# Optimization experiments

Measured on AMD Instinct MI355X. Metric: run time of the kernel, lower is better.

Reference implementation:

```python
import jax, jax.numpy as jnp
import numpy as np

V, D, E, N, Dd, Dc, NL, B, L = 50280, 1024, 2048, 16, 64, 4, 2, 2, 1024
EPS = 1e-5


def rmsnorm(x, w):
    return x * jax.lax.rsqrt(jnp.mean(x * x, axis=-1, keepdims=True) + EPS) * w


def setup_inputs() -> dict:
    key = jax.random.key(0)
    ks = jax.random.split(key, 18)
    n = jax.random.normal
    inp = {
        "input_ids": jax.random.randint(ks[0], (B, L), 0, V),
        "embedding": n(ks[1], (V, D), jnp.float32) * 0.02,
        "lm_head_w": n(ks[2], (V, D), jnp.float32) * 0.02,
        "norm_w": jnp.ones((D,), jnp.float32),
        # stacked per-layer params (leading dim = n_layer)
        "l_norm_w": jnp.ones((NL, D), jnp.float32),
        "l_skip_w": n(ks[3], (NL, E, D), jnp.float32) / np.sqrt(D),
        "l_in_w": n(ks[4], (NL, E, D), jnp.float32) / np.sqrt(D),
        "l_conv_w": n(ks[5], (NL, E, 1, Dc), jnp.float32) / np.sqrt(Dc),
        "l_conv_b": jnp.zeros((NL, E), jnp.float32),
        "l_Wd1": n(ks[6], (NL, Dd, E), jnp.float32) / np.sqrt(E),
        "l_Wd2_w": n(ks[7], (NL, E, Dd), jnp.float32) / np.sqrt(Dd),
        "l_Wd2_b": n(ks[8], (NL, E), jnp.float32) * 0.1 - 4.0,  # small dt init
        "l_WB": n(ks[9], (NL, N, E), jnp.float32) / np.sqrt(E),
        "l_WC": n(ks[10], (NL, N, E), jnp.float32) / np.sqrt(E),
        "l_A_log": jnp.log(jax.random.uniform(ks[11], (NL, E, N), jnp.float32, 0.5, 1.2)),
        "l_WD": jnp.ones((NL, E), jnp.float32),
        "l_out_w": n(ks[12], (NL, D, E), jnp.float32) / np.sqrt(E),
    }
    return inp


def mamba_layer(resid, norm_w, skip_w, in_w, conv_w, conv_b, Wd1, Wd2_w, Wd2_b,
                WB, WC, A_log, WD, out_w):
    x = rmsnorm(resid, norm_w)                      # [B,L,D]
    skip = x @ skip_w.T                             # [B,L,E]
    x = x @ in_w.T                                  # [B,L,E]
    # depthwise causal conv (pad D_conv-1 on left == pad both + slice [:L])
    xc = jax.lax.conv_general_dilated(
        x.transpose(0, 2, 1), conv_w, (1,), [(Dc - 1, 0)],
        feature_group_count=E, dimension_numbers=("NCH", "OIH", "NCH"))
    x = (xc + conv_b[None, :, None]).transpose(0, 2, 1)  # [B,L,E]
    x = jax.nn.silu(x)

    delta = jax.nn.softplus((x @ Wd1.T) @ Wd2_w.T + Wd2_b)  # [B,L,E]
    A = -jnp.exp(A_log)                                      # [E,N]
    A_bar = jnp.exp(delta[..., None] * A)                    # [B,L,E,N]
    Bt = x @ WB.T                                            # [B,L,N]
    Ct = x @ WC.T                                            # [B,L,N]
    Bx = (delta * x)[..., None] * Bt[:, :, None, :]          # [B,L,E,N]

    def step(h, inp):
        Ab_t, Bx_t, C_t = inp                                # [B,E,N],[B,E,N],[B,N]
        h = Ab_t * h + Bx_t
        y = jnp.einsum("ben,bn->be", h, C_t)
        return h, y

    h0 = jnp.zeros((B, E, N), x.dtype)
    _, ys = jax.lax.scan(step, h0,
                         (A_bar.transpose(1, 0, 2, 3), Bx.transpose(1, 0, 2, 3),
                          Ct.transpose(1, 0, 2)))
    y = ys.transpose(1, 0, 2)                                # [B,L,E]
    y = y + x * WD
    y = y * jax.nn.silu(skip)
    return resid + y @ out_w.T


def reference(input_ids, embedding, lm_head_w, norm_w, l_norm_w, l_skip_w, l_in_w,
              l_conv_w, l_conv_b, l_Wd1, l_Wd2_w, l_Wd2_b, l_WB, l_WC, l_A_log,
              l_WD, l_out_w):
    resid = embedding[input_ids]                             # [B,L,D]
    for i in range(NL):
        resid = mamba_layer(resid, l_norm_w[i], l_skip_w[i], l_in_w[i],
                            l_conv_w[i], l_conv_b[i], l_Wd1[i], l_Wd2_w[i],
                            l_Wd2_b[i], l_WB[i], l_WC[i], l_A_log[i], l_WD[i],
                            l_out_w[i])
    resid = rmsnorm(resid, norm_w)
    return resid @ lm_head_w.T                               # [B,L,V]
```

## Files before the change

### kernel.cpp

```cpp
#include <hip/hip_runtime.h>

typedef unsigned short u16;
using bf16x8 = __attribute__((ext_vector_type(8))) __bf16;
using f32x4  = __attribute__((ext_vector_type(4))) float;

typedef const void __attribute__((address_space(1))) gvoid_t;
typedef void __attribute__((address_space(3))) lvoid_t;

#define NL 2
#define Bd 2
#define Ld 1024
#define Dd_ 1024
#define Ed 2048
#define Nd 16
#define TOK (Bd*Ld)
#define VPAD 50432
#define VREAL 50280
#define NCHUNK 8
#define CLEN 128
#define XLD 4096

__device__ __forceinline__ u16 f2bf(float f) {
    union { float f; unsigned u; } v; v.f = f;
    unsigned u = v.u;
    unsigned r = (u + 0x7fffu + ((u >> 16) & 1u)) >> 16;
    return (u16)r;
}
__device__ __forceinline__ float siluf(float x) { return x / (1.f + __expf(-x)); }
__device__ __forceinline__ float softplusf(float z) {
    return (z > 15.f) ? z : log1pf(__expf(z));
}

__global__ void k_f32_to_bf16(const float* __restrict__ s, u16* __restrict__ d, int n4) {
    int i = blockIdx.x * 256 + threadIdx.x;
    if (i >= n4) return;
    float4 v = *(const float4*)&s[(size_t)i * 4];
    ushort4 o; o.x = f2bf(v.x); o.y = f2bf(v.y); o.z = f2bf(v.z); o.w = f2bf(v.w);
    *(ushort4*)&d[(size_t)i * 4] = o;
}

__global__ void k_f32_to_bf16_pad(const float* __restrict__ s, u16* __restrict__ d,
                                  int n4valid, int n4tot) {
    int i = blockIdx.x * 256 + threadIdx.x;
    if (i >= n4tot) return;
    ushort4 o;
    if (i < n4valid) {
        float4 v = *(const float4*)&s[(size_t)i * 4];
        o.x = f2bf(v.x); o.y = f2bf(v.y); o.z = f2bf(v.z); o.w = f2bf(v.w);
    } else { o.x = o.y = o.z = o.w = 0; }
    *(ushort4*)&d[(size_t)i * 4] = o;
}

__global__ void k_build_wsmall(const float* __restrict__ Wd1, const float* __restrict__ WB,
                               const float* __restrict__ WC, u16* __restrict__ dst) {
    int i = blockIdx.x * 256 + threadIdx.x;
    int col = (i * 4) & (Ed - 1);
    int r = (i * 4) >> 11;
    ushort4 o;
    const float* src = nullptr;
    if (r < 64) src = &Wd1[(size_t)r * Ed];
    else if (r < 80) src = &WB[(size_t)(r - 64) * Ed];
    else if (r < 96) src = &WC[(size_t)(r - 80) * Ed];
    if (src) {
        float4 v = *(const float4*)&src[col];
        o.x = f2bf(v.x); o.y = f2bf(v.y); o.z = f2bf(v.z); o.w = f2bf(v.w);
    } else { o.x = o.y = o.z = o.w = 0; }
    *(ushort4*)&dst[(size_t)i * 4] = o;
}

__global__ void k_embed(const int* __restrict__ ids, const float* __restrict__ emb,
                        float* __restrict__ resid) {
    int tk = blockIdx.x;
    int d = threadIdx.x * 4;
    int id = ids[tk];
    float4 v = *(const float4*)&emb[(size_t)id * Dd_ + d];
    *(float4*)&resid[(size_t)tk * Dd_ + d] = v;
}

__global__ void k_rmsnorm_bf16(const float* __restrict__ in, const float* __restrict__ w,
                               u16* __restrict__ out) {
    int tk = blockIdx.x;
    int tid = threadIdx.x;
    float4 v = *(const float4*)&in[(size_t)tk * Dd_ + tid * 4];
    float ss = v.x * v.x + v.y * v.y + v.z * v.z + v.w * v.w;
    #pragma unroll
    for (int m = 32; m; m >>= 1) ss += __shfl_xor(ss, m);
    __shared__ float red[4];
    if ((tid & 63) == 0) red[tid >> 6] = ss;
    __syncthreads();
    ss = red[0] + red[1] + red[2] + red[3];
    float rs = rsqrtf(ss * (1.f / 1024.f) + 1e-5f);
    float4 wv = *(const float4*)&w[tid * 4];
    ushort4 o;
    o.x = f2bf(v.x * rs * wv.x); o.y = f2bf(v.y * rs * wv.y);
    o.z = f2bf(v.z * rs * wv.z); o.w = f2bf(v.w * rs * wv.w);
    *(ushort4*)&out[(size_t)tk * Dd_ + tid * 4] = o;
}

__global__ void k_conv_silu(const float* __restrict__ xin, const float* __restrict__ cw,
                            const float* __restrict__ cb, float* __restrict__ xout,
                            u16* __restrict__ xbf) {
    int blk = blockIdx.x;
    int tk = blk >> 1;
    int e0 = ((blk & 1) << 10) + threadIdx.x * 4;
    int b = tk >> 10, l = tk & 1023;
    float4 w0 = *(const float4*)&cw[(size_t)(e0 + 0) * 4];
    float4 w1 = *(const float4*)&cw[(size_t)(e0 + 1) * 4];
    float4 w2 = *(const float4*)&cw[(size_t)(e0 + 2) * 4];
    float4 w3 = *(const float4*)&cw[(size_t)(e0 + 3) * 4];
    float4 bv = *(const float4*)&cb[e0];
    float a0 = bv.x, a1 = bv.y, a2 = bv.z, a3 = bv.w;
    const float* wp0 = (const float*)&w0; const float* wp1 = (const float*)&w1;
    const float* wp2 = (const float*)&w2; const float* wp3 = (const float*)&w3;
    #pragma unroll
    for (int k = 0; k < 4; ++k) {
        int ll = l - 3 + k;
        if (ll < 0) continue;
        float4 xv = *(const float4*)&xin[((size_t)(b * 1024 + ll)) * XLD + e0];
        a0 = fmaf(xv.x, wp0[k], a0); a1 = fmaf(xv.y, wp1[k], a1);
        a2 = fmaf(xv.z, wp2[k], a2); a3 = fmaf(xv.w, wp3[k], a3);
    }
    a0 = siluf(a0); a1 = siluf(a1); a2 = siluf(a2); a3 = siluf(a3);
    float4 o; o.x = a0; o.y = a1; o.z = a2; o.w = a3;
    *(float4*)&xout[(size_t)tk * Ed + e0] = o;
    ushort4 ob; ob.x = f2bf(a0); ob.y = f2bf(a1); ob.z = f2bf(a2); ob.w = f2bf(a3);
    *(ushort4*)&xbf[(size_t)tk * Ed + e0] = ob;
}

__global__ void k_reduce_xs(const float* __restrict__ part, float* __restrict__ xs,
                            u16* __restrict__ xsbf) {
    size_t i4 = ((size_t)blockIdx.x * 256 + threadIdx.x) * 4;
    float4 s = *(const float4*)&part[i4];
    #pragma unroll
    for (int c = 1; c < NCHUNK; ++c) {
        float4 v = *(const float4*)&part[(size_t)c * TOK * 128 + i4];
        s.x += v.x; s.y += v.y; s.z += v.z; s.w += v.w;
    }
    *(float4*)&xs[i4] = s;
    ushort4 o; o.x = f2bf(s.x); o.y = f2bf(s.y); o.z = f2bf(s.z); o.w = f2bf(s.w);
    *(ushort4*)&xsbf[i4] = o;
}

__global__ void k_scan_pass1(const float* __restrict__ delta, const float* __restrict__ x,
                             const float* __restrict__ xs, const float* __restrict__ A_log,
                             float* __restrict__ sumd, float* __restrict__ Hc) {
    int t = blockIdx.x * 256 + threadIdx.x;
    int n = t & 15;
    int gg = t >> 4;
    int e = gg & (Ed - 1);
    int cb = gg >> 11;
    int b = cb & 1, c = cb >> 1;
    float dA = -__expf(A_log[e * Nd + n]);
    float h = 0.f, sd = 0.f;
    size_t rowbase = ((size_t)b << 10) + c * CLEN;
    for (int l = 0; l < CLEN; ++l) {
        size_t row = rowbase + l;
        float dlt = delta[row * Ed + e];
        float xv  = x[row * Ed + e];
        float bt  = xs[row * 128 + 64 + n];
        float a = __expf(dA * dlt);
        h = fmaf(a, h, dlt * xv * bt);
        sd += dlt;
    }
    Hc[(size_t)gg * Nd + n] = h;
    if (n == 0) sumd[gg] = sd;
}

__global__ void k_scan_combine(const float* __restrict__ sumd, const float* __restrict__ Hc,
                               const float* __restrict__ A_log, float* __restrict__ Hin) {
    int idx = blockIdx.x * 256 + threadIdx.x;
    int n = idx & 15;
    int e = (idx >> 4) & (Ed - 1);
    int b = idx >> 15;
    float dA = -__expf(A_log[e * Nd + n]);
    float h = 0.f;
    #pragma unroll
    for (int c = 0; c < NCHUNK; ++c) {
        size_t g = ((size_t)(c * Bd + b) * Ed + e);
        Hin[g * Nd + n] = h;
        float a = __expf(dA * sumd[g]);
        h = fmaf(a, h, Hc[g * Nd + n]);
    }
}

__global__ void k_scan_pass2(const float* __restrict__ delta, const float* __restrict__ x,
                             const float* __restrict__ xs, const float* __restrict__ A_log,
                             const float* __restrict__ Hin, const float* __restrict__ WD,
                             const float* __restrict__ skipg, u16* __restrict__ ybf) {
    int t = blockIdx.x * 256 + threadIdx.x;
    int n = t & 15;
    int gg = t >> 4;
    int e = gg & (Ed - 1);
    int cb = gg >> 11;
    int b = cb & 1, c = cb >> 1;
    float dA = -__expf(A_log[e * Nd + n]);
    float h = Hin[(size_t)gg * Nd + n];
    float wd = WD[e];
    size_t rowbase = ((size_t)b << 10) + c * CLEN;
    for (int l = 0; l < CLEN; ++l) {
        size_t row = rowbase + l;
        float dlt = delta[row * Ed + e];
        float xv  = x[row * Ed + e];
        float bt  = xs[row * 128 + 64 + n];
        float ct  = xs[row * 128 + 80 + n];
        float a = __expf(dA * dlt);
        h = fmaf(a, h, dlt * xv * bt);
        float yv = h * ct;
        yv += __shfl_xor(yv, 1);
        yv += __shfl_xor(yv, 2);
        yv += __shfl_xor(yv, 4);
        yv += __shfl_xor(yv, 8);
        if (n == 0) {
            float yo = yv + xv * wd;
            float sk = skipg[row * XLD + e];
            ybf[row * Ed + e] = f2bf(yo * siluf(sk));
        }
    }
}

template<int EPI>
__global__ __launch_bounds__(256, 2)
void k_gemm_bt(const u16* __restrict__ A, int lda,
               const u16* __restrict__ B, int ldb,
               float* __restrict__ C, int ldc,
               const float* __restrict__ aux,
               int ntm, int Nstore, int Kc, size_t Cz) {
    __shared__ u16 lsA[2][128 * 32];
    __shared__ u16 lsB[2][128 * 32];
    int kz = blockIdx.z;
    A += (size_t)kz * Kc;
    B += (size_t)kz * Kc;
    C += (size_t)kz * Cz;
    int tid = threadIdx.x;
    int bid = blockIdx.x;
    int mt = bid % ntm, nt = bid / ntm;
    int mBase = mt * 128, nBase = nt * 128;
    int lane = tid & 63, wid = tid >> 6;
    int wr = wid >> 1, wc = wid & 1;

    f32x4 acc[4][4] = {};
    const u16* Ablk = A + (size_t)mBase * lda;
    const u16* Bblk = B + (size_t)nBase * ldb;
    int nk = Kc >> 5;

    auto stage = [&](int buf, int kt) {
        #pragma unroll
        for (int i = 0; i < 2; ++i) {
            int chunk = i * 256 + tid;
            int row = chunk >> 2;
            int kc  = (chunk & 3) << 3;
            const u16* ga = Ablk + (size_t)row * lda + (kt << 5) + kc;
            const u16* gb = Bblk + (size_t)row * ldb + (kt << 5) + kc;
            u16* la = &lsA[buf][(size_t)(i * 256 + wid * 64) * 8];
            u16* lb = &lsB[buf][(size_t)(i * 256 + wid * 64) * 8];
            __builtin_amdgcn_global_load_lds((gvoid_t*)ga, (lvoid_t*)la, 16, 0, 0);
            __builtin_amdgcn_global_load_lds((gvoid_t*)gb, (lvoid_t*)lb, 16, 0, 0);
        }
    };
    auto compute = [&](int buf) {
        bf16x8 af[4], bfr[4];
        const u16* baseA = lsA[buf];
        const u16* baseB = lsB[buf];
        int kq = (lane >> 4) << 3;
        int r  = lane & 15;
        #pragma unroll
        for (int mi = 0; mi < 4; ++mi)
            af[mi] = *(const bf16x8*)&baseA[(size_t)((wr * 64 + mi * 16 + r) * 32 + kq)];
        #pragma unroll
        for (int ni = 0; ni < 4; ++ni)
            bfr[ni] = *(const bf16x8*)&baseB[(size_t)((wc * 64 + ni * 16 + r) * 32 + kq)];
        #pragma unroll
        for (int mi = 0; mi < 4; ++mi)
            #pragma unroll
            for (int ni = 0; ni < 4; ++ni)
                acc[mi][ni] = __builtin_amdgcn_mfma_f32_16x16x32_bf16(af[mi], bfr[ni], acc[mi][ni], 0, 0, 0);
    };

    stage(0, 0);
    asm volatile("s_waitcnt vmcnt(0)" ::: "memory");
    __syncthreads();
    int cur = 0;
    for (int kt = 0; kt + 1 < nk; ++kt) {
        stage(cur ^ 1, kt + 1);
        compute(cur);
        asm volatile("s_waitcnt vmcnt(0)" ::: "memory");
        __syncthreads();
        cur ^= 1;
    }
    compute(cur);

    int rbase = (lane >> 4) * 4, ccol = lane & 15;
    #pragma unroll
    for (int mi = 0; mi < 4; ++mi) {
        #pragma unroll
        for (int ni = 0; ni < 4; ++ni) {
            int gc = nBase + wc * 64 + ni * 16 + ccol;
            if (gc < Nstore) {
                float bias = (EPI == 2) ? aux[gc] : 0.f;
                #pragma unroll
                for (int rr = 0; rr < 4; ++rr) {
                    int gr = mBase + wr * 64 + mi * 16 + rbase + rr;
                    size_t off = (size_t)gr * ldc + gc;
                    float v = acc[mi][ni][rr];
                    if (EPI == 1) v += aux[off];
                    if (EPI == 2) v = softplusf(v + bias);
                    C[off] = v;
                }
            }
        }
    }
}

#define BAR()    asm volatile("s_barrier" ::: "memory")
#define WAITV2() asm volatile("s_waitcnt vmcnt(2)" ::: "memory")
#define WAITV0() asm volatile("s_waitcnt vmcnt(0)" ::: "memory")

#define STG(buf, mat, h, kt) { \
    const u16* _s0 = ((mat) ? srcB[(h)*2]     : srcA[(h)*2])     + (size_t)(kt) * 64; \
    const u16* _s1 = ((mat) ? srcB[(h)*2 + 1] : srcA[(h)*2 + 1]) + (size_t)(kt) * 64; \
    char* _d = (char*)&ls[buf][mat][0]; \
    __builtin_amdgcn_global_load_lds((gvoid_t*)_s0, (lvoid_t*)(_d + (h)*16384 + tid*16), 16, 0, 0); \
    __builtin_amdgcn_global_load_lds((gvoid_t*)_s1, (lvoid_t*)(_d + (h)*16384 + 8192 + tid*16), 16, 0, 0); }

#define QUAD(buf, kk, mih) { \
    const char* _pa = (const char*)&ls[buf][0][0]; \
    const char* _pb = (const char*)&ls[buf][1][0]; \
    bf16x8 _af[4], _bf[4]; \
    _Pragma("unroll") \
    for (int _m = 0; _m < 4; ++_m) \
        _af[_m] = *(const bf16x8*)(_pa + abase + ((mih)*4 + _m) * 2048 + (kk) * 1024); \
    _Pragma("unroll") \
    for (int _n = 0; _n < 4; ++_n) \
        _bf[_n] = *(const bf16x8*)(_pb + bbase + _n * 2048 + (kk) * 1024); \
    __builtin_amdgcn_s_setprio(1); \
    _Pragma("unroll") \
    for (int _m = 0; _m < 4; ++_m) \
        _Pragma("unroll") \
        for (int _n = 0; _n < 4; ++_n) \
            acc[(mih)*4 + _m][_n] = __builtin_amdgcn_mfma_f32_16x16x32_bf16(_af[_m], _bf[_n], acc[(mih)*4 + _m][_n], 0, 0, 0); \
    __builtin_amdgcn_s_setprio(0); }

__global__ __launch_bounds__(512, 2)
void k_gemm256(const u16* __restrict__ A, int lda,
               const u16* __restrict__ B, int ldb,
               float* __restrict__ C, int ldc,
               int ntm, int Nstore, int K) {
    __shared__ u16 ls[2][2][256 * 64];
    const int tid = threadIdx.x;
    const int lane = tid & 63, wid = tid >> 6;
    const int wr = wid >> 2, wc = wid & 3;

    int nwg = gridDim.x, bid = blockIdx.x;
    int q8 = nwg >> 3, r8 = nwg & 7;
    int xcd = bid & 7, linb = bid >> 3;
    int sb = (xcd < r8 ? xcd * (q8 + 1) : r8 * (q8 + 1) + (xcd - r8) * q8) + linb;
    int mt = sb % ntm, nt = sb / ntm;

    const u16* Ablk = A + (size_t)(mt * 256) * lda;
    const u16* Bblk = B + (size_t)(nt * 256) * ldb;

    const u16* srcA[4]; const u16* srcB[4];
    #pragma unroll
    for (int s = 0; s < 4; ++s) {
        int p = s * 8192 + tid * 16;
        int qq = p ^ (((p >> 9) & 1) << 5);
        int sub = qq >> 10, rin = (qq >> 6) & 15, cby = qq & 63;
        int row = ((sub >> 1) << 4) | rin;
        int col = ((((sub & 1) << 6) | cby)) >> 1;
        srcA[s] = Ablk + (size_t)row * lda + col;
        srcB[s] = Bblk + (size_t)row * ldb + col;
    }
    int l15 = lane & 15;
    int lowb = (l15 * 64 + ((lane >> 4) << 4)) ^ (((l15 >> 3) & 1) << 5);
    int abase = wr * 16384 + lowb;
    int bbase = wc * 8192  + lowb;

    f32x4 acc[8][4] = {};
    int nk = K >> 6, nit = nk >> 1;

    STG(0, 0, 0, 0); STG(0, 0, 1, 0); STG(0, 1, 0, 0); STG(0, 1, 1, 0);

    for (int i = 0; i < nit; ++i) {
        int t1 = 2 * i + 1, t2 = 2 * i + 2;
        bool more = (i + 1 < nit);
        STG(1, 0, 0, t1);
        WAITV2(); BAR();
        QUAD(0, 0, 0); BAR();
        STG(1, 0, 1, t1);
        QUAD(0, 0, 1); BAR();
        STG(1, 1, 0, t1);
        QUAD(0, 1, 0); BAR();
        STG(1, 1, 1, t1);
        QUAD(0, 1, 1); BAR();
        if (more) { STG(0, 0, 0, t2); WAITV2(); } else { WAITV0(); }
        BAR();
        QUAD(1, 0, 0); BAR();
        if (more) STG(0, 0, 1, t2);
        QUAD(1, 0, 1); BAR();
        if (more) STG(0, 1, 0, t2);
        QUAD(1, 1, 0); BAR();
        if (more) STG(0, 1, 1, t2);
        QUAD(1, 1, 1); BAR();
    }

    int rb = (lane >> 4) * 4, cc = lane & 15;
    int mrow = mt * 256 + wr * 128, ncol = nt * 256 + wc * 64;
    #pragma unroll
    for (int mi = 0; mi < 8; ++mi) {
        #pragma unroll
        for (int ni = 0; ni < 4; ++ni) {
            int gc = ncol + ni * 16 + cc;
            if (gc < Nstore) {
                #pragma unroll
                for (int rr = 0; rr < 4; ++rr) {
                    size_t off = (size_t)(mrow + mi * 16 + rb + rr) * ldc + gc;
                    C[off] = acc[mi][ni][rr];
                }
            }
        }
    }
}

extern "C" void kernel_launch(void* const* d_in, const int* in_sizes, int n_in,
                              void* d_out, int out_size, void* d_ws, size_t ws_size,
                              hipStream_t stream) {
    const int*   ids   = (const int*)d_in[0];
    const float* emb   = (const float*)d_in[1];
    const float* lmw   = (const float*)d_in[2];
    const float* normw = (const float*)d_in[3];
    const float* lnw   = (const float*)d_in[4];
    const float* lskip = (const float*)d_in[5];
    const float* linw  = (const float*)d_in[6];
    const float* lcw   = (const float*)d_in[7];
    const float* lcb   = (const float*)d_in[8];
    const float* lWd1  = (const float*)d_in[9];
    const float* lWd2  = (const float*)d_in[10];
    const float* lWd2b = (const float*)d_in[11];
    const float* lWB   = (const float*)d_in[12];
    const float* lWC   = (const float*)d_in[13];
    const float* lAlog = (const float*)d_in[14];
    const float* lWD   = (const float*)d_in[15];
    const float* loutw = (const float*)d_in[16];
    float* out = (float*)d_out;

    char* ws = (char*)d_ws;
    size_t off = 0;
    auto alloc = [&](size_t bytes) { char* p = ws + off; off += (bytes + 255) & ~(size_t)255; return p; };
    u16*   lm_bf    = (u16*)  alloc((size_t)VPAD * 1024 * 2);
    u16*   wsi_bf   = (u16*)  alloc((size_t)NL * 4096 * Dd_ * 2);
    u16*   wout_bf  = (u16*)  alloc((size_t)NL * Dd_ * Ed * 2);
    u16*   wd2_bf   = (u16*)  alloc((size_t)NL * Ed * 64 * 2);
    u16*   wsml_bf  = (u16*)  alloc((size_t)NL * 128 * Ed * 2);
    float* resid    = (float*)alloc((size_t)TOK * Dd_ * 4);
    u16*   xn_bf    = (u16*)  alloc((size_t)TOK * Dd_ * 2);
    float* xall     = (float*)alloc((size_t)TOK * XLD * 4);
    float* xf       = (float*)alloc((size_t)TOK * Ed * 4);
    u16*   xbf      = (u16*)  alloc((size_t)TOK * Ed * 2);
    float* xs       = (float*)alloc((size_t)TOK * 128 * 4);
    u16*   xs_bf    = (u16*)  alloc((size_t)TOK * 128 * 2);
    float* xs_part  = (float*)alloc((size_t)NCHUNK * TOK * 128 * 4);
    float* delta    = (float*)alloc((size_t)TOK * Ed * 4);
    float* sumd     = (float*)alloc((size_t)NCHUNK * Bd * Ed * 4);
    float* Hc       = (float*)alloc((size_t)NCHUNK * Bd * Ed * Nd * 4);
    float* Hin      = (float*)alloc((size_t)NCHUNK * Bd * Ed * Nd * 4);
    u16*   ybf      = (u16*)  alloc((size_t)TOK * Ed * 2);
    (void)ws_size; (void)in_sizes; (void)n_in; (void)out_size;

    {
        int n4v = VREAL * 1024 / 4, n4t = VPAD * 1024 / 4;
        k_f32_to_bf16_pad<<<(n4t + 255) / 256, 256, 0, stream>>>(lmw, lm_bf, n4v, n4t);
        int n4 = Ed * Dd_ / 4;
        for (int lyr = 0; lyr < NL; ++lyr) {
            k_f32_to_bf16<<<(n4 + 255) / 256, 256, 0, stream>>>(
                lskip + (size_t)lyr * Ed * Dd_, wsi_bf + (size_t)lyr * 4096 * Dd_, n4);
            k_f32_to_bf16<<<(n4 + 255) / 256, 256, 0, stream>>>(
                linw + (size_t)lyr * Ed * Dd_, wsi_bf + (size_t)lyr * 4096 * Dd_ + (size_t)Ed * Dd_, n4);
        }
        k_f32_to_bf16<<<(NL * n4 + 255) / 256, 256, 0, stream>>>(loutw, wout_bf, NL * n4);
        int n4b = NL * Ed * 64 / 4;
        k_f32_to_bf16<<<(n4b + 255) / 256, 256, 0, stream>>>(lWd2, wd2_bf, n4b);
        for (int lyr = 0; lyr < NL; ++lyr)
            k_build_wsmall<<<256, 256, 0, stream>>>(lWd1 + (size_t)lyr * 64 * Ed,
                                                    lWB + (size_t)lyr * Nd * Ed,
                                                    lWC + (size_t)lyr * Nd * Ed,
                                                    wsml_bf + (size_t)lyr * 128 * Ed);
    }

    k_embed<<<TOK, 256, 0, stream>>>(ids, emb, resid);

    for (int lyr = 0; lyr < NL; ++lyr) {
        const float* Alog = lAlog + (size_t)lyr * Ed * Nd;
        k_rmsnorm_bf16<<<TOK, 256, 0, stream>>>(resid, lnw + (size_t)lyr * Dd_, xn_bf);
        k_gemm_bt<0><<<dim3(16 * 32, 1, 1), 256, 0, stream>>>(xn_bf, Dd_,
            wsi_bf + (size_t)lyr * 4096 * Dd_, Dd_, xall, XLD, nullptr, 16, 4096, 1024, 0);
        k_conv_silu<<<TOK * 2, 256, 0, stream>>>(xall + Ed, lcw + (size_t)lyr * Ed * 4,
                                                 lcb + (size_t)lyr * Ed, xf, xbf);
        k_gemm_bt<0><<<dim3(16, 1, NCHUNK), 256, 0, stream>>>(xbf, Ed,
            wsml_bf + (size_t)lyr * 128 * Ed, Ed, xs_part, 128, nullptr, 16, 128, 256,
            (size_t)TOK * 128);
        k_reduce_xs<<<TOK * 128 / 4 / 256, 256, 0, stream>>>(xs_part, xs, xs_bf);
        k_gemm_bt<2><<<dim3(16 * 16, 1, 1), 256, 0, stream>>>(xs_bf, 128,
            wd2_bf + (size_t)lyr * Ed * 64, 64, delta, Ed, lWd2b + (size_t)lyr * Ed,
            16, Ed, 64, 0);
        k_scan_pass1<<<NCHUNK * Bd * Ed * Nd / 256, 256, 0, stream>>>(delta, xf, xs, Alog, sumd, Hc);
        k_scan_combine<<<Bd * Ed * Nd / 256, 256, 0, stream>>>(sumd, Hc, Alog, Hin);
        k_scan_pass2<<<NCHUNK * Bd * Ed * Nd / 256, 256, 0, stream>>>(delta, xf, xs, Alog, Hin,
            lWD + (size_t)lyr * Ed, xall, ybf);
        k_gemm_bt<1><<<dim3(16 * 8, 1, 1), 256, 0, stream>>>(ybf, Ed,
            wout_bf + (size_t)lyr * Dd_ * Ed, Ed, resid, Dd_, resid, 16, Dd_, 2048, 0);
    }

    k_rmsnorm_bf16<<<TOK, 256, 0, stream>>>(resid, normw, xn_bf);
    k_gemm256<<<dim3(8 * (VPAD / 256), 1, 1), 512, 0, stream>>>(xn_bf, Dd_, lm_bf, Dd_,
        out, VREAL, 8, VREAL, 1024);
}
```

Baseline: 943.2 us.

## Restructure selective scan to one thread per channel and reshape lm_head pipeline

The scan kernels switch from sixteen threads per channel, which reduced the output with shuffles, to one thread per channel that keeps all 16 state values in registers. Each block stages B/C rows in shared memory, and the chunk count doubles to 16 chunks of 64 steps to keep enough threads in flight. The xs split-K reduction is decoupled and stays at 8. Separately, the big lm_head GEMM's inner loop now issues twice as many LDS loads and MFMAs per stage between barriers, with a looser vmcnt wait. This cuts barrier count but raises register pressure.

```diff
diff --git a/kernel.cpp b/kernel.cpp
--- a/kernel.cpp
+++ b/kernel.cpp
@@ -16,8 +16,8 @@
 #define TOK (Bd*Ld)
 #define VPAD 50432
 #define VREAL 50280
-#define NCHUNK 8
-#define CLEN 128
+#define NCHUNK 16
+#define CLEN 64
 #define XLD 4096
 
 __device__ __forceinline__ u16 f2bf(float f) {
@@ -132,7 +132,7 @@
     size_t i4 = ((size_t)blockIdx.x * 256 + threadIdx.x) * 4;
     float4 s = *(const float4*)&part[i4];
     #pragma unroll
-    for (int c = 1; c < NCHUNK; ++c) {
+    for (int c = 1; c < 8; ++c) {
         float4 v = *(const float4*)&part[(size_t)c * TOK * 128 + i4];
         s.x += v.x; s.y += v.y; s.z += v.z; s.w += v.w;
     }
@@ -144,26 +144,47 @@
 __global__ void k_scan_pass1(const float* __restrict__ delta, const float* __restrict__ x,
                              const float* __restrict__ xs, const float* __restrict__ A_log,
                              float* __restrict__ sumd, float* __restrict__ Hc) {
+    __shared__ float sBt[CLEN][16];
     int t = blockIdx.x * 256 + threadIdx.x;
-    int n = t & 15;
-    int gg = t >> 4;
-    int e = gg & (Ed - 1);
-    int cb = gg >> 11;
+    int e = t & (Ed - 1);
+    int cb = t >> 11;
     int b = cb & 1, c = cb >> 1;
-    float dA = -__expf(A_log[e * Nd + n]);
-    float h = 0.f, sd = 0.f;
-    size_t rowbase = ((size_t)b << 10) + c * CLEN;
+    int rowbase = b * 1024 + c * CLEN;
+    {
+        int f = threadIdx.x * 4;
+        int row = f >> 4, cc = f & 15;
+        float4 v = *(const float4*)&xs[(size_t)(rowbase + row) * 128 + 64 + cc];
+        *(float4*)&sBt[row][cc] = v;
+    }
+    __syncthreads();
+    float dA[16], h[16];
+    #pragma unroll
+    for (int n = 0; n < 16; ++n) { dA[n] = -__expf(A_log[e * 16 + n]); h[n] = 0.f; }
+    float sd = 0.f;
     for (int l = 0; l < CLEN; ++l) {
-        size_t row = rowbase + l;
+        size_t row = (size_t)rowbase + l;
         float dlt = delta[row * Ed + e];
         float xv  = x[row * Ed + e];
-        float bt  = xs[row * 128 + 64 + n];
-        float a = __expf(dA * dlt);
-        h = fmaf(a, h, dlt * xv * bt);
         sd += dlt;
-    }
-    Hc[(size_t)gg * Nd + n] = h;
-    if (n == 0) sumd[gg] = sd;
+        float dx = dlt * xv;
+        float4 bt0 = *(const float4*)&sBt[l][0];
+        float4 bt1 = *(const float4*)&sBt[l][4];
+        float4 bt2 = *(const float4*)&sBt[l][8];
+        float4 bt3 = *(const float4*)&sBt[l][12];
+        const float* btp = (const float*)&bt0;
+        float bts[16] = {bt0.x,bt0.y,bt0.z,bt0.w, bt1.x,bt1.y,bt1.z,bt1.w,
+                         bt2.x,bt2.y,bt2.z,bt2.w, bt3.x,bt3.y,bt3.z,bt3.w};
+        (void)btp;
+        #pragma unroll
+        for (int n = 0; n < 16; ++n) {
+            float a = __expf(dA[n] * dlt);
+            h[n] = fmaf(a, h[n], dx * bts[n]);
+        }
+    }
+    size_t gg = (size_t)cb * Ed + e;
+    #pragma unroll
+    for (int n = 0; n < 16; ++n) Hc[gg * 16 + n] = h[n];
+    sumd[gg] = sd;
 }
 
 __global__ void k_scan_combine(const float* __restrict__ sumd, const float* __restrict__ Hc,
@@ -187,34 +208,56 @@
                              const float* __restrict__ xs, const float* __restrict__ A_log,
                              const float* __restrict__ Hin, const float* __restrict__ WD,
                              const float* __restrict__ skipg, u16* __restrict__ ybf) {
+    __shared__ float sBC[CLEN][32];
     int t = blockIdx.x * 256 + threadIdx.x;
-    int n = t & 15;
-    int gg = t >> 4;
-    int e = gg & (Ed - 1);
-    int cb = gg >> 11;
+    int e = t & (Ed - 1);
+    int cb = t >> 11;
     int b = cb & 1, c = cb >> 1;
-    float dA = -__expf(A_log[e * Nd + n]);
-    float h = Hin[(size_t)gg * Nd + n];
+    int rowbase = b * 1024 + c * CLEN;
+    {
+        int f = threadIdx.x * 8;
+        int row = f >> 5, cc = f & 31;
+        float4 v0 = *(const float4*)&xs[(size_t)(rowbase + row) * 128 + 64 + cc];
+        float4 v1 = *(const float4*)&xs[(size_t)(rowbase + row) * 128 + 64 + cc + 4];
+        *(float4*)&sBC[row][cc] = v0;
+        *(float4*)&sBC[row][cc + 4] = v1;
+    }
+    __syncthreads();
+    float dA[16], h[16];
+    size_t gg = (size_t)cb * Ed + e;
+    #pragma unroll
+    for (int n = 0; n < 16; ++n) {
+        dA[n] = -__expf(A_log[e * 16 + n]);
+        h[n] = Hin[gg * 16 + n];
+    }
     float wd = WD[e];
-    size_t rowbase = ((size_t)b << 10) + c * CLEN;
     for (int l = 0; l < CLEN; ++l) {
-        size_t row = rowbase + l;
+        size_t row = (size_t)rowbase + l;
         float dlt = delta[row * Ed + e];
         float xv  = x[row * Ed + e];
-        float bt  = xs[row * 128 + 64 + n];
-        float ct  = xs[row * 128 + 80 + n];
-        float a = __expf(dA * dlt);
-        h = fmaf(a, h, dlt * xv * bt);
-        float yv = h * ct;
-        yv += __shfl_xor(yv, 1);
-        yv += __shfl_xor(yv, 2);
-        yv += __shfl_xor(yv, 4);
-        yv += __shfl_xor(yv, 8);
-        if (n == 0) {
-            float yo = yv + xv * wd;
-            float sk = skipg[row * XLD + e];
-            ybf[row * Ed + e] = f2bf(yo * siluf(sk));
+        float dx = dlt * xv;
+        float4 b0 = *(const float4*)&sBC[l][0];
+        float4 b1 = *(const float4*)&sBC[l][4];
+        float4 b2 = *(const float4*)&sBC[l][8];
+        float4 b3 = *(const float4*)&sBC[l][12];
+        float4 c0 = *(const float4*)&sBC[l][16];
+        float4 c1 = *(const float4*)&sBC[l][20];
+        float4 c2 = *(const float4*)&sBC[l][24];
+        float4 c3 = *(const float4*)&sBC[l][28];
+        float bts[16] = {b0.x,b0.y,b0.z,b0.w, b1.x,b1.y,b1.z,b1.w,
+                         b2.x,b2.y,b2.z,b2.w, b3.x,b3.y,b3.z,b3.w};
+        float cts[16] = {c0.x,c0.y,c0.z,c0.w, c1.x,c1.y,c1.z,c1.w,
+                         c2.x,c2.y,c2.z,c2.w, c3.x,c3.y,c3.z,c3.w};
+        float y = 0.f;
+        #pragma unroll
+        for (int n = 0; n < 16; ++n) {
+            float a = __expf(dA[n] * dlt);
+            h[n] = fmaf(a, h[n], dx * bts[n]);
+            y = fmaf(h[n], cts[n], y);
         }
+        float yo = y + xv * wd;
+        float sk = skipg[row * XLD + e];
+        ybf[row * Ed + e] = f2bf(yo * siluf(sk));
     }
 }
 
@@ -312,7 +355,7 @@
 }
 
 #define BAR()    asm volatile("s_barrier" ::: "memory")
-#define WAITV2() asm volatile("s_waitcnt vmcnt(2)" ::: "memory")
+#define WAITV4() asm volatile("s_waitcnt vmcnt(4)" ::: "memory")
 #define WAITV0() asm volatile("s_waitcnt vmcnt(0)" ::: "memory")
 
 #define STG(buf, mat, h, kt) { \
@@ -322,22 +365,22 @@
     __builtin_amdgcn_global_load_lds((gvoid_t*)_s0, (lvoid_t*)(_d + (h)*16384 + tid*16), 16, 0, 0); \
     __builtin_amdgcn_global_load_lds((gvoid_t*)_s1, (lvoid_t*)(_d + (h)*16384 + 8192 + tid*16), 16, 0, 0); }
 
-#define QUAD(buf, kk, mih) { \
+#define KSLICE(buf, kk) { \
     const char* _pa = (const char*)&ls[buf][0][0]; \
     const char* _pb = (const char*)&ls[buf][1][0]; \
-    bf16x8 _af[4], _bf[4]; \
+    bf16x8 _af[8], _bf[4]; \
     _Pragma("unroll") \
-    for (int _m = 0; _m < 4; ++_m) \
-        _af[_m] = *(const bf16x8*)(_pa + abase + ((mih)*4 + _m) * 2048 + (kk) * 1024); \
+    for (int _m = 0; _m < 8; ++_m) \
+        _af[_m] = *(const bf16x8*)(_pa + abase + _m * 2048 + (kk) * 1024); \
     _Pragma("unroll") \
     for (int _n = 0; _n < 4; ++_n) \
         _bf[_n] = *(const bf16x8*)(_pb + bbase + _n * 2048 + (kk) * 1024); \
     __builtin_amdgcn_s_setprio(1); \
     _Pragma("unroll") \
-    for (int _m = 0; _m < 4; ++_m) \
+    for (int _m = 0; _m < 8; ++_m) \
         _Pragma("unroll") \
         for (int _n = 0; _n < 4; ++_n) \
-            acc[(mih)*4 + _m][_n] = __builtin_amdgcn_mfma_f32_16x16x32_bf16(_af[_m], _bf[_n], acc[(mih)*4 + _m][_n], 0, 0, 0); \
+            acc[_m][_n] = __builtin_amdgcn_mfma_f32_16x16x32_bf16(_af[_m], _bf[_n], acc[_m][_n], 0, 0, 0); \
     __builtin_amdgcn_s_setprio(0); }
 
 __global__ __launch_bounds__(512, 2)
@@ -383,24 +426,16 @@
     for (int i = 0; i < nit; ++i) {
         int t1 = 2 * i + 1, t2 = 2 * i + 2;
         bool more = (i + 1 < nit);
-        STG(1, 0, 0, t1);
-        WAITV2(); BAR();
-        QUAD(0, 0, 0); BAR();
-        STG(1, 0, 1, t1);
-        QUAD(0, 0, 1); BAR();
-        STG(1, 1, 0, t1);
-        QUAD(0, 1, 0); BAR();
-        STG(1, 1, 1, t1);
-        QUAD(0, 1, 1); BAR();
-        if (more) { STG(0, 0, 0, t2); WAITV2(); } else { WAITV0(); }
+        STG(1, 0, 0, t1); STG(1, 0, 1, t1);
+        WAITV4(); BAR();
+        KSLICE(0, 0); BAR();
+        STG(1, 1, 0, t1); STG(1, 1, 1, t1);
+        KSLICE(0, 1); BAR();
+        if (more) { STG(0, 0, 0, t2); STG(0, 0, 1, t2); WAITV4(); } else { WAITV0(); }
         BAR();
-        QUAD(1, 0, 0); BAR();
-        if (more) STG(0, 0, 1, t2);
-        QUAD(1, 0, 1); BAR();
-        if (more) STG(0, 1, 0, t2);
-        QUAD(1, 1, 0); BAR();
-        if (more) STG(0, 1, 1, t2);
-        QUAD(1, 1, 1); BAR();
+        KSLICE(1, 0); BAR();
+        if (more) { STG(0, 1, 0, t2); STG(0, 1, 1, t2); }
+        KSLICE(1, 1); BAR();
     }
 
     int rb = (lane >> 4) * 4, cc = lane & 15;
@@ -458,7 +493,7 @@
     u16*   xbf      = (u16*)  alloc((size_t)TOK * Ed * 2);
     float* xs       = (float*)alloc((size_t)TOK * 128 * 4);
     u16*   xs_bf    = (u16*)  alloc((size_t)TOK * 128 * 2);
-    float* xs_part  = (float*)alloc((size_t)NCHUNK * TOK * 128 * 4);
+    float* xs_part  = (float*)alloc((size_t)8 * TOK * 128 * 4);
     float* delta    = (float*)alloc((size_t)TOK * Ed * 4);
     float* sumd     = (float*)alloc((size_t)NCHUNK * Bd * Ed * 4);
     float* Hc       = (float*)alloc((size_t)NCHUNK * Bd * Ed * Nd * 4);
@@ -495,16 +530,16 @@
             wsi_bf + (size_t)lyr * 4096 * Dd_, Dd_, xall, XLD, nullptr, 16, 4096, 1024, 0);
         k_conv_silu<<<TOK * 2, 256, 0, stream>>>(xall + Ed, lcw + (size_t)lyr * Ed * 4,
                                                  lcb + (size_t)lyr * Ed, xf, xbf);
-        k_gemm_bt<0><<<dim3(16, 1, NCHUNK), 256, 0, stream>>>(xbf, Ed,
+        k_gemm_bt<0><<<dim3(16, 1, 8), 256, 0, stream>>>(xbf, Ed,
             wsml_bf + (size_t)lyr * 128 * Ed, Ed, xs_part, 128, nullptr, 16, 128, 256,
             (size_t)TOK * 128);
         k_reduce_xs<<<TOK * 128 / 4 / 256, 256, 0, stream>>>(xs_part, xs, xs_bf);
         k_gemm_bt<2><<<dim3(16 * 16, 1, 1), 256, 0, stream>>>(xs_bf, 128,
             wd2_bf + (size_t)lyr * Ed * 64, 64, delta, Ed, lWd2b + (size_t)lyr * Ed,
             16, Ed, 64, 0);
-        k_scan_pass1<<<NCHUNK * Bd * Ed * Nd / 256, 256, 0, stream>>>(delta, xf, xs, Alog, sumd, Hc);
+        k_scan_pass1<<<NCHUNK * Bd * Ed / 256, 256, 0, stream>>>(delta, xf, xs, Alog, sumd, Hc);
         k_scan_combine<<<Bd * Ed * Nd / 256, 256, 0, stream>>>(sumd, Hc, Alog, Hin);
-        k_scan_pass2<<<NCHUNK * Bd * Ed * Nd / 256, 256, 0, stream>>>(delta, xf, xs, Alog, Hin,
+        k_scan_pass2<<<NCHUNK * Bd * Ed / 256, 256, 0, stream>>>(delta, xf, xs, Alog, Hin,
             lWD + (size_t)lyr * Ed, xall, ybf);
         k_gemm_bt<1><<<dim3(16 * 8, 1, 1), 256, 0, stream>>>(ybf, Ed,
             wout_bf + (size_t)lyr * Dd_ * Ed, Ed, resid, Dd_, resid, 16, Dd_, 2048, 0);
```

New measurement: 1.129 ms. +19.7%, slower.
